# Optimization experiments

Measured on AMD Instinct MI355X. Metric: run time of the kernel, lower is better.

The kernel has to match this reference:

```python
import jax, jax.numpy as jnp
import numpy as np

B, N, D, H, O, K, N_USER, C = 1, 4096, 64, 4, 64, 2, 4000, 2


def setup_inputs() -> dict:
    key = jax.random.key(0)
    ks = jax.random.split(key, 7)
    h = jax.random.normal(ks[0], (B, N, D), jnp.float32)
    # dense 0/1 adjacency per heterogeneous kind, with self-loops so no row is empty
    adj = jax.random.randint(ks[1], (K, B, N, N), 0, 2).astype(jnp.float32)
    hadj = jnp.maximum(adj, jnp.eye(N, dtype=jnp.float32))
    s = 1.0 / np.sqrt(D).astype(np.float32)
    w = jax.random.normal(ks[2], (K, H, D, O), jnp.float32) * s
    a_src = jax.random.normal(ks[3], (K, H, O, 1), jnp.float32) * (1.0 / np.sqrt(O).astype(np.float32))
    a_dst = jax.random.normal(ks[4], (K, H, O, 1), jnp.float32) * (1.0 / np.sqrt(O).astype(np.float32))
    fc_w = jax.random.normal(ks[5], (C, O * K), jnp.float32) * (1.0 / np.sqrt(O * K).astype(np.float32))
    fc_b = jnp.zeros((C,), jnp.float32)
    return {"h": h, "hadj": hadj, "w": w, "a_src": a_src, "a_dst": a_dst, "fc_w": fc_w, "fc_b": fc_b}


def _gat(h, adj, w_k, a_src_k, a_dst_k):
    # h: (B,N,D); adj: (B,N,N); w_k: (H,D,O); a_*: (H,O,1)
    h_prime = jnp.einsum('bnf,hfo->bhno', h, w_k)          # (B,H,N,O)
    t = jnp.tanh(h_prime)
    attn_src = jnp.einsum('bhno,hoi->bhni', t, a_src_k)    # (B,H,N,1)
    attn_dst = jnp.einsum('bhno,hoi->bhni', t, a_dst_k)    # (B,H,N,1)
    attn = attn_src + jnp.swapaxes(attn_dst, -1, -2)       # (B,H,N,N) broadcast add
    attn = jnp.where(attn >= 0, attn, 0.2 * attn)          # LeakyReLU(0.2)
    attn = jnp.where(adj[:, None] > 0, attn, -jnp.inf)     # dense mask
    attn = jax.nn.softmax(attn, axis=-1)                   # dropout is a no-op in eval
    out = jnp.einsum('bhnm,bhmo->bhno', attn, h_prime)     # (B,H,N,O)
    return out.mean(axis=1)                                # mean over heads -> (B,N,O)


def reference(h, hadj, w, a_src, a_dst, fc_w, fc_b):
    embs = []
    for k in range(K):  # small fixed loop over heterogeneous node kinds
        x = _gat(h, hadj[k], w[k], a_src[k], a_dst[k])
        embs.append(x[:, :N_USER])
    type_aware = jnp.concatenate(embs, axis=-1)            # (B, N_USER, K*O)
    logits = type_aware @ fc_w.T + fc_b                    # (B, N_USER, C)
    return jax.nn.log_softmax(logits, axis=-1)
```

## Files before the change

kernel.cpp:

```cpp
#include <hip/hip_runtime.h>
#include <math.h>

constexpr int KK = 2;
constexpr int HH = 4;
constexpr int NN = 4096;
constexpr int DD = 64;
constexpr int OO = 64;
constexpr int NU = 4000;
constexpr int CC = 2;
constexpr int JSPLIT = 8;
constexpr int JCHUNK = NN / JSPLIT;
constexpr int NTILE = JCHUNK / 16;
constexpr float LOG2E = 1.44269504088896340736f;

typedef float vf4 __attribute__((ext_vector_type(4)));

__device__ __forceinline__ float fexp2(float x) {
#if __has_builtin(__builtin_amdgcn_exp2f)
  return __builtin_amdgcn_exp2f(x);
#else
  return exp2f(x);
#endif
}
__device__ __forceinline__ float frcp(float x) {
#if __has_builtin(__builtin_amdgcn_rcpf)
  return __builtin_amdgcn_rcpf(x);
#else
  return 1.0f / x;
#endif
}
__device__ __forceinline__ float ftanh(float x) {
  float e = fexp2(x * (2.0f * LOG2E));
  return 1.0f - 2.0f * frcp(e + 1.0f);
}

__global__ __launch_bounds__(256) void gat_phase1(
    const float* __restrict__ hsrc, const float* __restrict__ w,
    const float* __restrict__ a_src, const float* __restrict__ a_dst,
    const float* __restrict__ fc_w,
    float* __restrict__ src_s, float* __restrict__ att_d,
    float* __restrict__ att_g0, float* __restrict__ att_g1) {
  const int kh = blockIdx.y;
  const int k = kh >> 2;
  const int i0 = blockIdx.x * 64;
  const int tid = threadIdx.x;

  __shared__ float h_s[DD][68];
  __shared__ float w_s[DD][OO];

  {
    const float4* wp = (const float4*)(w + (size_t)kh * DD * OO);
    float4* ws4 = (float4*)w_s;
    for (int t = tid; t < DD * OO / 4; t += 256) ws4[t] = wp[t];
  }
  for (int t = tid; t < 1024; t += 256) {
    const int row = t >> 4;
    const int f4 = (t & 15) * 4;
    float4 v = *(const float4*)(hsrc + (size_t)(i0 + row) * DD + f4);
    h_s[f4 + 0][row] = v.x;
    h_s[f4 + 1][row] = v.y;
    h_s[f4 + 2][row] = v.z;
    h_s[f4 + 3][row] = v.w;
  }
  __syncthreads();

  const int og = tid & 15;
  const int rg = tid >> 4;
  const int o0 = og * 4;
  const int r0 = rg * 4;

  float hp[4][4];
#pragma unroll
  for (int j = 0; j < 4; ++j)
#pragma unroll
    for (int u = 0; u < 4; ++u) hp[j][u] = 0.0f;

#pragma unroll 8
  for (int f = 0; f < DD; ++f) {
    float4 hv = *(const float4*)&h_s[f][r0];
    float4 wv = *(const float4*)&w_s[f][o0];
    hp[0][0] = fmaf(hv.x, wv.x, hp[0][0]);
    hp[0][1] = fmaf(hv.x, wv.y, hp[0][1]);
    hp[0][2] = fmaf(hv.x, wv.z, hp[0][2]);
    hp[0][3] = fmaf(hv.x, wv.w, hp[0][3]);
    hp[1][0] = fmaf(hv.y, wv.x, hp[1][0]);
    hp[1][1] = fmaf(hv.y, wv.y, hp[1][1]);
    hp[1][2] = fmaf(hv.y, wv.z, hp[1][2]);
    hp[1][3] = fmaf(hv.y, wv.w, hp[1][3]);
    hp[2][0] = fmaf(hv.z, wv.x, hp[2][0]);
    hp[2][1] = fmaf(hv.z, wv.y, hp[2][1]);
    hp[2][2] = fmaf(hv.z, wv.z, hp[2][2]);
    hp[2][3] = fmaf(hv.z, wv.w, hp[2][3]);
    hp[3][0] = fmaf(hv.w, wv.x, hp[3][0]);
    hp[3][1] = fmaf(hv.w, wv.y, hp[3][1]);
    hp[3][2] = fmaf(hv.w, wv.z, hp[3][2]);
    hp[3][3] = fmaf(hv.w, wv.w, hp[3][3]);
  }

  float as[4], ad[4], f0[4], f1[4];
#pragma unroll
  for (int u = 0; u < 4; ++u) {
    as[u] = a_src[kh * OO + o0 + u];
    ad[u] = a_dst[kh * OO + o0 + u];
    f0[u] = fc_w[0 * (KK * OO) + k * OO + o0 + u];
    f1[u] = fc_w[1 * (KK * OO) + k * OO + o0 + u];
  }

#pragma unroll
  for (int j = 0; j < 4; ++j) {
    float sp = 0.0f, dp = 0.0f, g0 = 0.0f, g1 = 0.0f;
#pragma unroll
    for (int u = 0; u < 4; ++u) {
      float v = hp[j][u];
      float t = ftanh(v);
      sp = fmaf(t, as[u], sp);
      dp = fmaf(t, ad[u], dp);
      g0 = fmaf(v, f0[u], g0);
      g1 = fmaf(v, f1[u], g1);
    }
#pragma unroll
    for (int off = 1; off < 16; off <<= 1) {
      sp += __shfl_xor(sp, off, 64);
      dp += __shfl_xor(dp, off, 64);
      g0 += __shfl_xor(g0, off, 64);
      g1 += __shfl_xor(g1, off, 64);
    }
    if (og == 0) {
      const int i = i0 + r0 + j;
      src_s[kh * NN + i] = sp * LOG2E;
      att_d[kh * NN + i] = dp * LOG2E;
      att_g0[kh * NN + i] = g0;
      att_g1[kh * NN + i] = g1;
    }
  }
}

__global__ __launch_bounds__(256) void gat_phase2(
    const float* __restrict__ adj, const float* __restrict__ src_s,
    const float* __restrict__ att_d, const float* __restrict__ att_g0,
    const float* __restrict__ att_g1, float* __restrict__ P) {
  const int k = blockIdx.y >> 3;
  const int chunk = blockIdx.y & 7;
  const int r0 = blockIdx.x * 16;
  const int tid = threadIdx.x;
  const int wave = tid >> 6;
  const int lane = tid & 63;
  const int row = lane & 15;
  const int jsub = lane >> 4;
  const int i = r0 + row;
  const int j0 = chunk * JCHUNK;

  __shared__ float lds_att[12][JCHUNK];
  {
    const float* planes[3] = {att_d, att_g0, att_g1};
#pragma unroll
    for (int step = 0; step < 6; ++step) {
      const int fi = step * 256 + tid;
      const int v = fi >> 7;
      const int pos = (fi & 127) * 4;
      const int p = v >> 2, h = v & 3;
      vf4 val = *(const vf4*)(planes[p] + (size_t)(k * HH + h) * NN + j0 + pos);
      *(vf4*)&lds_att[v][pos] = val;
    }
  }

  float sreg[4];
#pragma unroll
  for (int h = 0; h < 4; ++h) sreg[h] = src_s[(k * HH + h) * NN + i];

  float l[4], a0[4], a1[4];
#pragma unroll
  for (int h = 0; h < 4; ++h) {
    l[h] = 0.0f;
    a0[h] = 0.0f;
    a1[h] = 0.0f;
  }

  __syncthreads();

  const float* arow = adj + (size_t)k * NN * NN + (size_t)i * NN + j0 + jsub * 4;
  vf4 apre0 = *(const vf4*)(arow + (wave + 0) * 16);
  vf4 apre1 = *(const vf4*)(arow + (wave + 4) * 16);

#pragma unroll
  for (int s = 0; s < 8; ++s) {
    const int t = wave + s * 4;
    const vf4 av = apre0;
    apre0 = apre1;
    if (s < 6) apre1 = *(const vf4*)(arow + (t + 8) * 16);
    const int jloc = jsub * 4 + t * 16;
#pragma unroll
    for (int h = 0; h < 4; ++h) {
      vf4 dv = *(const vf4*)&lds_att[0 * 4 + h][jloc];
      vf4 g0v = *(const vf4*)&lds_att[1 * 4 + h][jloc];
      vf4 g1v = *(const vf4*)&lds_att[2 * 4 + h][jloc];
#pragma unroll
      for (int jj = 0; jj < 4; ++jj) {
        float s2 = sreg[h] + dv[jj];
        float sl = fmaxf(s2, 0.2f * s2);
        float p = av[jj] * fexp2(sl);
        l[h] += p;
        a0[h] = fmaf(p, g0v[jj], a0[h]);
        a1[h] = fmaf(p, g1v[jj], a1[h]);
      }
    }
  }

#pragma unroll
  for (int h = 0; h < 4; ++h) {
    l[h] += __shfl_xor(l[h], 16, 64);
    l[h] += __shfl_xor(l[h], 32, 64);
    a0[h] += __shfl_xor(a0[h], 16, 64);
    a0[h] += __shfl_xor(a0[h], 32, 64);
    a1[h] += __shfl_xor(a1[h], 16, 64);
    a1[h] += __shfl_xor(a1[h], 32, 64);
  }

  __shared__ float sred[4][12][16];
  if (lane < 16) {
#pragma unroll
    for (int h = 0; h < 4; ++h) {
      sred[wave][h * 3 + 0][row] = l[h];
      sred[wave][h * 3 + 1][row] = a0[h];
      sred[wave][h * 3 + 2][row] = a1[h];
    }
  }
  __syncthreads();
  if (tid < 192) {
    const int v = tid >> 4;
    const int rr = tid & 15;
    float sum =
        sred[0][v][rr] + sred[1][v][rr] + sred[2][v][rr] + sred[3][v][rr];
    const int h = v / 3, c = v % 3;
    size_t base =
        ((((size_t)(k * JSPLIT + chunk) * HH + h) * 3 + c)) * NU + (r0 + rr);
    P[base] = sum;
  }
}

__global__ __launch_bounds__(256) void gat_phase3(
    const float* __restrict__ P, const float* __restrict__ fc_b,
    float* __restrict__ out) {
  const int i = blockIdx.x * 256 + threadIdx.x;
  if (i >= NU) return;
  float l0 = fc_b[0], l1 = fc_b[1];
#pragma unroll
  for (int k = 0; k < KK; ++k) {
#pragma unroll
    for (int q = 0; q < HH; ++q) {
      float ls = 0.0f, a0 = 0.0f, a1 = 0.0f;
#pragma unroll
      for (int ch = 0; ch < JSPLIT; ++ch) {
        size_t b = (((size_t)(k * JSPLIT + ch) * HH + q) * 3) * NU + i;
        ls += P[b];
        a0 += P[b + NU];
        a1 += P[b + 2 * (size_t)NU];
      }
      float inv = 1.0f / ls;
      l0 = fmaf(0.25f * a0, inv, l0);
      l1 = fmaf(0.25f * a1, inv, l1);
    }
  }
  float m = fmaxf(l0, l1);
  float lse = m + logf(expf(l0 - m) + expf(l1 - m));
  out[i * CC + 0] = l0 - lse;
  out[i * CC + 1] = l1 - lse;
}

extern "C" void kernel_launch(void* const* d_in, const int* in_sizes, int n_in,
                              void* d_out, int out_size, void* d_ws, size_t ws_size,
                              hipStream_t stream) {
  const float* hsrc  = (const float*)d_in[0];
  const float* hadj  = (const float*)d_in[1];
  const float* w     = (const float*)d_in[2];
  const float* a_src = (const float*)d_in[3];
  const float* a_dst = (const float*)d_in[4];
  const float* fc_w  = (const float*)d_in[5];
  const float* fc_b  = (const float*)d_in[6];
  float* out = (float*)d_out;

  char* ws = (char*)d_ws;
  float* src_s  = (float*)(ws + 0 * 131072);
  float* att_d  = (float*)(ws + 1 * 131072);
  float* att_g0 = (float*)(ws + 2 * 131072);
  float* att_g1 = (float*)(ws + 3 * 131072);
  float* P      = (float*)(ws + 4 * 131072);

  dim3 g1(NN / 64, KK * HH);
  gat_phase1<<<g1, 256, 0, stream>>>(hsrc, w, a_src, a_dst, fc_w,
                                     src_s, att_d, att_g0, att_g1);
  dim3 g2(NU / 16, KK * JSPLIT);
  gat_phase2<<<g2, 256, 0, stream>>>(hadj, src_s, att_d, att_g0, att_g1, P);
  gat_phase3<<<(NU + 255) / 256, 256, 0, stream>>>(P, fc_b, out);
}
```

Before: 222.7 us.

## Pack phase2 math into float2 ops, deepen adj prefetch, LDS-reduce phase1

Phase 2's inner softmax-accumulate loop now works on float2 pairs so the compiler can emit packed FP32 instructions (add, mul, fma, max). The adjacency prefetch grows from two to four vf4 loads in flight, and the src_s load is hoisted ahead of the LDS staging. Phase 1 swaps the 16-lane shuffle reductions for an LDS partial-sum table reduced with vector loads by all threads. The aim is to cut VALU instruction count and hide global-load latency, at the cost of more registers and extra LDS.

```diff
diff --git a/kernel.cpp b/kernel.cpp
--- a/kernel.cpp
+++ b/kernel.cpp
@@ -10,10 +10,10 @@
 constexpr int CC = 2;
 constexpr int JSPLIT = 8;
 constexpr int JCHUNK = NN / JSPLIT;
-constexpr int NTILE = JCHUNK / 16;
 constexpr float LOG2E = 1.44269504088896340736f;
 
 typedef float vf4 __attribute__((ext_vector_type(4)));
+typedef float vf2 __attribute__((ext_vector_type(2)));
 
 __device__ __forceinline__ float fexp2(float x) {
 #if __has_builtin(__builtin_amdgcn_exp2f)
@@ -47,16 +47,17 @@
 
   __shared__ float h_s[DD][68];
   __shared__ float w_s[DD][OO];
+  __shared__ float part[4][64][17];
 
   {
-    const float4* wp = (const float4*)(w + (size_t)kh * DD * OO);
-    float4* ws4 = (float4*)w_s;
+    const vf4* wp = (const vf4*)(w + (size_t)kh * DD * OO);
+    vf4* ws4 = (vf4*)w_s;
     for (int t = tid; t < DD * OO / 4; t += 256) ws4[t] = wp[t];
   }
   for (int t = tid; t < 1024; t += 256) {
     const int row = t >> 4;
     const int f4 = (t & 15) * 4;
-    float4 v = *(const float4*)(hsrc + (size_t)(i0 + row) * DD + f4);
+    vf4 v = *(const vf4*)(hsrc + (size_t)(i0 + row) * DD + f4);
     h_s[f4 + 0][row] = v.x;
     h_s[f4 + 1][row] = v.y;
     h_s[f4 + 2][row] = v.z;
@@ -77,8 +78,8 @@
 
 #pragma unroll 8
   for (int f = 0; f < DD; ++f) {
-    float4 hv = *(const float4*)&h_s[f][r0];
-    float4 wv = *(const float4*)&w_s[f][o0];
+    vf4 hv = *(const vf4*)&h_s[f][r0];
+    vf4 wv = *(const vf4*)&w_s[f][o0];
     hp[0][0] = fmaf(hv.x, wv.x, hp[0][0]);
     hp[0][1] = fmaf(hv.x, wv.y, hp[0][1]);
     hp[0][2] = fmaf(hv.x, wv.z, hp[0][2]);
@@ -118,20 +119,27 @@
       g0 = fmaf(v, f0[u], g0);
       g1 = fmaf(v, f1[u], g1);
     }
-#pragma unroll
-    for (int off = 1; off < 16; off <<= 1) {
-      sp += __shfl_xor(sp, off, 64);
-      dp += __shfl_xor(dp, off, 64);
-      g0 += __shfl_xor(g0, off, 64);
-      g1 += __shfl_xor(g1, off, 64);
-    }
-    if (og == 0) {
-      const int i = i0 + r0 + j;
-      src_s[kh * NN + i] = sp * LOG2E;
-      att_d[kh * NN + i] = dp * LOG2E;
-      att_g0[kh * NN + i] = g0;
-      att_g1[kh * NN + i] = g1;
-    }
+    part[0][r0 + j][og] = sp;
+    part[1][r0 + j][og] = dp;
+    part[2][r0 + j][og] = g0;
+    part[3][r0 + j][og] = g1;
+  }
+  __syncthreads();
+
+  {
+    const int val = tid & 3;
+    const int j2 = tid >> 2;
+    const float* pr = &part[val][j2][0];
+    vf4 s0 = *(const vf4*)(pr + 0);
+    vf4 s1 = *(const vf4*)(pr + 4);
+    vf4 s2 = *(const vf4*)(pr + 8);
+    vf4 s3 = *(const vf4*)(pr + 12);
+    vf4 t4 = s0 + s1 + s2 + s3;
+    float sum = t4.x + t4.y + t4.z + t4.w;
+    if (val < 2) sum *= LOG2E;
+    float* base = (val == 0) ? src_s : (val == 1) ? att_d
+                 : (val == 2) ? att_g0 : att_g1;
+    base[kh * NN + i0 + j2] = sum;
   }
 }
 
@@ -150,6 +158,14 @@
   const int i = r0 + row;
   const int j0 = chunk * JCHUNK;
 
+  vf2 sreg2[4];
+#pragma unroll
+  for (int h = 0; h < 4; ++h) {
+    float s = src_s[(k * HH + h) * NN + i];
+    sreg2[h].x = s;
+    sreg2[h].y = s;
+  }
+
   __shared__ float lds_att[12][JCHUNK];
   {
     const float* planes[3] = {att_d, att_g0, att_g1};
@@ -164,30 +180,28 @@
     }
   }
 
-  float sreg[4];
-#pragma unroll
-  for (int h = 0; h < 4; ++h) sreg[h] = src_s[(k * HH + h) * NN + i];
-
-  float l[4], a0[4], a1[4];
+  vf2 l2[4], a02[4], a12[4];
 #pragma unroll
   for (int h = 0; h < 4; ++h) {
-    l[h] = 0.0f;
-    a0[h] = 0.0f;
-    a1[h] = 0.0f;
+    l2[h] = (vf2)(0.0f);
+    a02[h] = (vf2)(0.0f);
+    a12[h] = (vf2)(0.0f);
   }
 
   __syncthreads();
 
-  const float* arow = adj + (size_t)k * NN * NN + (size_t)i * NN + j0 + jsub * 4;
-  vf4 apre0 = *(const vf4*)(arow + (wave + 0) * 16);
-  vf4 apre1 = *(const vf4*)(arow + (wave + 4) * 16);
+  const float* arow =
+      adj + (size_t)k * NN * NN + (size_t)i * NN + j0 + jsub * 4;
+  vf4 apre[4];
+#pragma unroll
+  for (int q = 0; q < 4; ++q)
+    apre[q] = *(const vf4*)(arow + (wave + q * 4) * 16);
 
 #pragma unroll
   for (int s = 0; s < 8; ++s) {
     const int t = wave + s * 4;
-    const vf4 av = apre0;
-    apre0 = apre1;
-    if (s < 6) apre1 = *(const vf4*)(arow + (t + 8) * 16);
+    const vf4 av = apre[s & 3];
+    if (s < 4) apre[s & 3] = *(const vf4*)(arow + (wave + (s + 4) * 4) * 16);
     const int jloc = jsub * 4 + t * 16;
 #pragma unroll
     for (int h = 0; h < 4; ++h) {
@@ -195,19 +209,30 @@
       vf4 g0v = *(const vf4*)&lds_att[1 * 4 + h][jloc];
       vf4 g1v = *(const vf4*)&lds_att[2 * 4 + h][jloc];
 #pragma unroll
-      for (int jj = 0; jj < 4; ++jj) {
-        float s2 = sreg[h] + dv[jj];
-        float sl = fmaxf(s2, 0.2f * s2);
-        float p = av[jj] * fexp2(sl);
-        l[h] += p;
-        a0[h] = fmaf(p, g0v[jj], a0[h]);
-        a1[h] = fmaf(p, g1v[jj], a1[h]);
+      for (int pp = 0; pp < 2; ++pp) {
+        vf2 dpair = {dv[2 * pp], dv[2 * pp + 1]};
+        vf2 apair = {av[2 * pp], av[2 * pp + 1]};
+        vf2 g0p = {g0v[2 * pp], g0v[2 * pp + 1]};
+        vf2 g1p = {g1v[2 * pp], g1v[2 * pp + 1]};
+        vf2 s2 = sreg2[h] + dpair;
+        vf2 sl = __builtin_elementwise_max(s2, s2 * 0.2f);
+        vf2 e;
+        e.x = fexp2(sl.x);
+        e.y = fexp2(sl.y);
+        vf2 p2 = apair * e;
+        l2[h] += p2;
+        a02[h] = __builtin_elementwise_fma(p2, g0p, a02[h]);
+        a12[h] = __builtin_elementwise_fma(p2, g1p, a12[h]);
       }
     }
   }
 
+  float l[4], a0[4], a1[4];
 #pragma unroll
   for (int h = 0; h < 4; ++h) {
+    l[h] = l2[h].x + l2[h].y;
+    a0[h] = a02[h].x + a02[h].y;
+    a1[h] = a12[h].x + a12[h].y;
     l[h] += __shfl_xor(l[h], 16, 64);
     l[h] += __shfl_xor(l[h], 32, 64);
     a0[h] += __shfl_xor(a0[h], 16, 64);
```

Measured after the change: 225.3 us. Within noise of the previous version (+1.1%).
